# Performance work log

Hardware: AMD Instinct MI355X
Metric: run time of the kernel (lower is better)

## Reference

```python
import jax, jax.numpy as jnp
import numpy as np

N = 50000  # nodes
E = 1600000  # directed edges
F_IN = 64
H = 64
C = 16
EPS = 1e-12


def setup_inputs() -> dict:
    key = jax.random.key(0)
    ks = jax.random.split(key, 10)
    x = jax.random.normal(ks[0], (N, F_IN), jnp.float32)
    edge_index = jax.random.randint(ks[1], (2, E), 0, N, dtype=jnp.int32)
    def lin(k, fan_in, fan_out):
        return jax.random.normal(k, (fan_in, fan_out), jnp.float32) * (1.0 / np.sqrt(fan_in))
    return {
        "x": x,
        "edge_index": edge_index,
        "W1": lin(ks[2], F_IN, H), "b1": jnp.zeros((H,), jnp.float32),
        "W2": lin(ks[3], H, H),    "b2": jnp.zeros((H,), jnp.float32),
        "W3": lin(ks[4], H, H),    "b3": jnp.zeros((H,), jnp.float32),
        "Wlin": lin(ks[5], 3 * H, C), "blin": jnp.zeros((C,), jnp.float32),
    }


def _gcn_norm(edge_index, n):
    # add self loops, compute symmetric GCN normalization D^-1/2 (A+I) D^-1/2
    loop = jnp.arange(n, dtype=edge_index.dtype)
    row = jnp.concatenate([edge_index[0], loop])  # target nodes
    col = jnp.concatenate([edge_index[1], loop])  # source nodes
    deg = jax.ops.segment_sum(jnp.ones_like(row, dtype=jnp.float32), row, num_segments=n)
    dis = jnp.where(deg > 0, jax.lax.rsqrt(jnp.maximum(deg, 1.0)), 0.0)
    norm = dis[row] * dis[col]  # [E+N]
    return row, col, norm


def _gcn_layer(x, row, col, norm, W, b):
    h = x @ W                              # [N, H]
    msg = h[col] * norm[:, None]           # gather sources, scale
    agg = jax.ops.segment_sum(msg, row, num_segments=x.shape[0])  # scatter-add
    return agg + b


def _l2norm(x):
    # torch F.normalize(p=2, dim=1)
    n = jnp.sqrt(jnp.sum(x * x, axis=1, keepdims=True))
    return x / jnp.maximum(n, EPS)


def reference(x, edge_index, W1, b1, W2, b2, W3, b3, Wlin, blin):
    row, col, norm = _gcn_norm(edge_index, x.shape[0])
    stack = []
    h = x
    for (W, b) in ((W1, b1), (W2, b2), (W3, b3)):
        h = _gcn_layer(h, row, col, norm, W, b)
        h = jax.nn.relu(h)
        h = _l2norm(h)
        stack.append(h)
    emb = jnp.concatenate(stack, axis=1)   # [N, 3H]
    out = emb @ Wlin + blin                # [N, C]
    return jax.nn.log_softmax(out, axis=1)
```

## Files before the change

### kernel.cpp

```cpp
#include <hip/hip_runtime.h>
#include <hip/hip_bf16.h>

#define NN 50000
#define NPAD 50048
#define EE 1600000
#define NB 391
#define CAPB 4608
#define CPAD 16
#define EPB 4096
#define BCAP 28

typedef __attribute__((ext_vector_type(8))) short short8;
typedef __attribute__((ext_vector_type(4))) float floatx4;

__device__ __forceinline__ float ldext(const void* p, long i, int f32) {
    return f32 ? ((const float*)p)[i]
               : __bfloat162float(((const __hip_bfloat16*)p)[i]);
}

__device__ __forceinline__ float b2f(unsigned short u) {
    unsigned int x = ((unsigned int)u) << 16;
    float f; __builtin_memcpy(&f, &x, 4); return f;
}
__device__ __forceinline__ unsigned short f2b(float f) {
    __hip_bfloat16 h = __float2bfloat16(f);
    unsigned short u; __builtin_memcpy(&u, &h, 2); return u;
}
__device__ __forceinline__ float asf(unsigned int x) {
    float f; __builtin_memcpy(&f, &x, 4); return f;
}

__global__ void k_bucket(const int* __restrict__ row, const int* __restrict__ col,
                         int* __restrict__ bcur, unsigned int* __restrict__ bdata,
                         const unsigned short* __restrict__ xu, int* __restrict__ flag) {
    __shared__ int lcnt[NB];
    __shared__ unsigned binned[NB * BCAP];
    __shared__ int dcnt;
    int tid = threadIdx.x;
    if (blockIdx.x == 0) {
        if (tid == 0) dcnt = 0;
        __syncthreads();
        int local = 0;
        for (int j = 0; j < 16; ++j) {
            unsigned short u = xu[2 * (tid + 256 * j)];
            int ex = (u >> 7) & 0xFF;
            if (ex == 0xFF || ex < 0x60) local++;
        }
        atomicAdd(&dcnt, local);
        __syncthreads();
        if (tid == 0) flag[0] = (dcnt > 256) ? 1 : 0;
    }
    long base = (long)blockIdx.x * EPB;
    int nedge = (int)min((long)EPB, (long)EE - base);
    for (int k = tid; k < NB; k += 256) lcnt[k] = 0;
    __syncthreads();
    const int4* r4 = (const int4*)(row + base);
    const int4* c4 = (const int4*)(col + base);
    for (int j = tid; j < (nedge >> 2); j += 256) {
        int4 rr = r4[j], cc = c4[j];
        #pragma unroll
        for (int t = 0; t < 4; ++t) {
            int r = (&rr.x)[t], c = (&cc.x)[t];
            int b = r >> 7;
            unsigned rec = ((unsigned)(r & 127) << 16) | (unsigned)c;
            int p = atomicAdd(&lcnt[b], 1);
            if (p < BCAP) binned[b * BCAP + p] = rec;
            else {
                int gp = atomicAdd(&bcur[b * CPAD], 1);
                if (gp < CAPB) bdata[(long)b * CAPB + gp] = rec;
            }
        }
    }
    __syncthreads();
    for (int b = tid; b < NB; b += 256) {
        int n = min(lcnt[b], BCAP);
        if (!n) continue;
        int gb = atomicAdd(&bcur[b * CPAD], n);
        long dst = (long)b * CAPB;
        for (int j = 0; j < n; ++j)
            if (gb + j < CAPB) bdata[dst + gb + j] = binned[b * BCAP + j];
    }
}

__global__ void k_csr(const int* __restrict__ bcur, const unsigned* __restrict__ bdata,
                      int* __restrict__ row_ptr, float* __restrict__ dis,
                      unsigned short* __restrict__ csr_col) {
    __shared__ unsigned recs[CAPB];
    __shared__ int cnt[128];
    __shared__ int incl[128];
    __shared__ int curs[128];
    __shared__ int redu[4];
    int b = blockIdx.x, tid = threadIdx.x;
    int lane = tid & 63, wid = tid >> 6;
    int part = 0;
    for (int j = tid; j < b; j += 256) part += min(bcur[j * CPAD], CAPB);
    #pragma unroll
    for (int off = 32; off; off >>= 1) part += __shfl_xor(part, off);
    if (lane == 0) redu[wid] = part;
    if (tid < 128) cnt[tid] = 0;
    __syncthreads();
    int base = redu[0] + redu[1] + redu[2] + redu[3];
    int n = min(bcur[b * CPAD], CAPB);
    const unsigned* dp = bdata + (long)b * CAPB;
    for (int i = tid; i < n; i += 256) {
        unsigned rec = dp[i];
        recs[i] = rec;
        atomicAdd(&cnt[(rec >> 16) & 127], 1);
    }
    __syncthreads();
    if (tid < 128) {
        int x = cnt[tid];
        #pragma unroll
        for (int off = 1; off < 64; off <<= 1) {
            int y = __shfl_up(x, off);
            if (lane >= off) x += y;
        }
        incl[tid] = x;
    }
    __syncthreads();
    int r0 = b << 7;
    if (tid < 128) {
        int ic = incl[tid] + (wid == 1 ? incl[63] : 0);
        int excl = base + ic - cnt[tid];
        curs[tid] = excl;
        int r = r0 + tid;
        if (r <= NN) row_ptr[r] = excl;
        if (r < NN) dis[r] = rsqrtf((float)(cnt[tid] + 1));
    }
    __syncthreads();
    for (int i = tid; i < n; i += 256) {
        unsigned rec = recs[i];
        int p = atomicAdd(&curs[(rec >> 16) & 127], 1);
        csr_col[p] = (unsigned short)(rec & 0xFFFF);
    }
}

template <bool EXT>
__global__ void k_gemm(const void* __restrict__ X, const void* __restrict__ W,
                       const int* __restrict__ flag, const float* __restrict__ dis,
                       unsigned short* __restrict__ Hout) {
    __shared__ __align__(16) unsigned short xs[64 * 72];
    int tid = threadIdx.x;
    int n0 = blockIdx.x * 64;
    const int f32 = flag[0];
    for (int idx = tid; idx < 4096; idx += 256) {
        int nn = idx >> 6, k = idx & 63;
        int n = n0 + nn;
        unsigned short v = 0;
        if (n < NN) {
            long ofs = (long)n * 64 + k;
            if (EXT) v = f32 ? f2b(((const float*)X)[ofs]) : ((const unsigned short*)X)[ofs];
            else     v = ((const unsigned short*)X)[ofs];
        }
        xs[nn * 72 + k] = v;
    }
    __syncthreads();
    int lane = tid & 63, wid = tid >> 6;
    int m0 = wid * 16;
    int quad = lane >> 4, nl = lane & 15;
    short8 a0 = *(const short8*)(xs + (m0 + nl) * 72 + quad * 8);
    short8 a1 = *(const short8*)(xs + (m0 + nl) * 72 + quad * 8 + 32);
    floatx4 acc[4];
    const unsigned short* Wb = (const unsigned short*)W;
    const float* Wf = (const float*)W;
    #pragma unroll
    for (int ct = 0; ct < 4; ++ct) {
        short8 b0, b1;
        int n = ct * 16 + nl;
        #pragma unroll
        for (int j = 0; j < 8; ++j) {
            int k0 = quad * 8 + j;
            b0[j] = (short)(f32 ? f2b(Wf[k0 * 64 + n]) : Wb[k0 * 64 + n]);
            b1[j] = (short)(f32 ? f2b(Wf[(k0 + 32) * 64 + n]) : Wb[(k0 + 32) * 64 + n]);
        }
        floatx4 c = {0.f, 0.f, 0.f, 0.f};
        c = __builtin_amdgcn_mfma_f32_16x16x32_bf16(a0, b0, c, 0, 0, 0);
        c = __builtin_amdgcn_mfma_f32_16x16x32_bf16(a1, b1, c, 0, 0, 0);
        acc[ct] = c;
    }
    #pragma unroll
    for (int r = 0; r < 4; ++r) {
        int node = n0 + m0 + quad * 4 + r;
        if (node < NN) {
            float dn = dis[node];
            #pragma unroll
            for (int ct = 0; ct < 4; ++ct)
                Hout[(long)node * 64 + ct * 16 + nl] = f2b(dn * acc[ct][r]);
        } else {
            #pragma unroll
            for (int ct = 0; ct < 4; ++ct)
                Hout[(long)node * 64 + ct * 16 + nl] = 0;
        }
    }
}

__global__ void k_agg(const uint4* __restrict__ hp128, const int* __restrict__ row_ptr,
                      const unsigned short* __restrict__ csr_col,
                      const float* __restrict__ dis, const void* __restrict__ bias,
                      const int* __restrict__ flag,
                      unsigned short* __restrict__ eo ) {
    int lane = threadIdx.x & 63, wid = threadIdx.x >> 6;
    int half = lane >> 5;
    int i = blockIdx.x * 8 + wid * 2 + half;
    bool valid = (i < NN);
    int iv = valid ? i : 0;
    int q4 = (lane >> 3) & 3;
    int fl = lane & 7;
    float2 A0 = {0,0}, A1 = {0,0}, A2 = {0,0}, A3 = {0,0};
    #define ADDU(u) do { \
        A0.x += asf((u).x << 16); A0.y += asf((u).x & 0xFFFF0000u); \
        A1.x += asf((u).y << 16); A1.y += asf((u).y & 0xFFFF0000u); \
        A2.x += asf((u).z << 16); A2.y += asf((u).z & 0xFFFF0000u); \
        A3.x += asf((u).w << 16); A3.y += asf((u).w & 0xFFFF0000u); } while (0)
    if (valid && q4 == 0) {
        uint4 u = hp128[(long)iv * 8 + fl];
        ADDU(u);
    }
    int e  = valid ? row_ptr[iv] : 0;
    int e1 = valid ? row_ptr[iv + 1] : 0;
    while (e < e1) {
        int i0 = e + q4,      i1 = e + 4 + q4,  i2 = e + 8 + q4,  i3 = e + 12 + q4;
        int i4 = e + 16 + q4, i5 = e + 20 + q4, i6 = e + 24 + q4, i7 = e + 28 + q4;
        int c0 = (i0 < e1) ? (int)csr_col[i0] : NN;
        int c1 = (i1 < e1) ? (int)csr_col[i1] : NN;
        int c2 = (i2 < e1) ? (int)csr_col[i2] : NN;
        int c3 = (i3 < e1) ? (int)csr_col[i3] : NN;
        int c4 = (i4 < e1) ? (int)csr_col[i4] : NN;
        int c5 = (i5 < e1) ? (int)csr_col[i5] : NN;
        int c6 = (i6 < e1) ? (int)csr_col[i6] : NN;
        int c7 = (i7 < e1) ? (int)csr_col[i7] : NN;
        uint4 u0 = hp128[(long)c0 * 8 + fl];
        uint4 u1 = hp128[(long)c1 * 8 + fl];
        uint4 u2 = hp128[(long)c2 * 8 + fl];
        uint4 u3 = hp128[(long)c3 * 8 + fl];
        uint4 u4 = hp128[(long)c4 * 8 + fl];
        uint4 u5 = hp128[(long)c5 * 8 + fl];
        uint4 u6 = hp128[(long)c6 * 8 + fl];
        uint4 u7 = hp128[(long)c7 * 8 + fl];
        ADDU(u0); ADDU(u1); ADDU(u2); ADDU(u3);
        ADDU(u4); ADDU(u5); ADDU(u6); ADDU(u7);
        e += 32;
    }
    #undef ADDU
    #pragma unroll
    for (int off = 8; off < 32; off <<= 1) {
        A0.x += __shfl_xor(A0.x, off); A0.y += __shfl_xor(A0.y, off);
        A1.x += __shfl_xor(A1.x, off); A1.y += __shfl_xor(A1.y, off);
        A2.x += __shfl_xor(A2.x, off); A2.y += __shfl_xor(A2.y, off);
        A3.x += __shfl_xor(A3.x, off); A3.y += __shfl_xor(A3.y, off);
    }
    const int f32 = flag[0];
    float di = dis[iv];
    float v0 = fmaf(di, A0.x, ldext(bias, 8 * fl + 0, f32));
    float v1 = fmaf(di, A0.y, ldext(bias, 8 * fl + 1, f32));
    float v2 = fmaf(di, A1.x, ldext(bias, 8 * fl + 2, f32));
    float v3 = fmaf(di, A1.y, ldext(bias, 8 * fl + 3, f32));
    float v4 = fmaf(di, A2.x, ldext(bias, 8 * fl + 4, f32));
    float v5 = fmaf(di, A2.y, ldext(bias, 8 * fl + 5, f32));
    float v6 = fmaf(di, A3.x, ldext(bias, 8 * fl + 6, f32));
    float v7 = fmaf(di, A3.y, ldext(bias, 8 * fl + 7, f32));
    v0 = fmaxf(v0, 0.f); v1 = fmaxf(v1, 0.f); v2 = fmaxf(v2, 0.f); v3 = fmaxf(v3, 0.f);
    v4 = fmaxf(v4, 0.f); v5 = fmaxf(v5, 0.f); v6 = fmaxf(v6, 0.f); v7 = fmaxf(v7, 0.f);
    float s = fmaf(v0, v0, fmaf(v1, v1, fmaf(v2, v2, v3 * v3)))
            + fmaf(v4, v4, fmaf(v5, v5, fmaf(v6, v6, v7 * v7)));
    #pragma unroll
    for (int off = 4; off; off >>= 1) s += __shfl_xor(s, off);
    float inv = 1.f / fmaxf(sqrtf(s), 1e-12f);
    if (valid && q4 == 0) {
        union { unsigned short us[8]; uint4 v; } pk;
        pk.us[0] = f2b(v0 * inv); pk.us[1] = f2b(v1 * inv);
        pk.us[2] = f2b(v2 * inv); pk.us[3] = f2b(v3 * inv);
        pk.us[4] = f2b(v4 * inv); pk.us[5] = f2b(v5 * inv);
        pk.us[6] = f2b(v6 * inv); pk.us[7] = f2b(v7 * inv);
        *(uint4*)(eo + (long)i * 64 + 8 * fl) = pk.v;
    }
}

__global__ void k_out(const unsigned short* __restrict__ emb, const void* __restrict__ Wlin,
                      const void* __restrict__ blin, const int* __restrict__ flag,
                      void* __restrict__ out) {
    int tid = threadIdx.x, lane = tid & 63, wid = tid >> 6;
    int quad = lane >> 4, nl = lane & 15;
    int base = blockIdx.x * 64 + wid * 16;
    const int f32 = flag[0];
    const unsigned short* Wb = (const unsigned short*)Wlin;
    const float* Wf = (const float*)Wlin;
    int ia = min(base + nl, NN - 1);
    floatx4 c = {0.f, 0.f, 0.f, 0.f};
    #pragma unroll
    for (int kc = 0; kc < 6; ++kc) {
        short8 b;
        #pragma unroll
        for (int j = 0; j < 8; ++j) {
            int k = kc * 32 + quad * 8 + j;
            b[j] = (short)(f32 ? f2b(Wf[k * 16 + nl]) : Wb[k * 16 + nl]);
        }
        int L = kc >> 1, ko = (kc & 1) * 32 + quad * 8;
        short8 a = *(const short8*)(emb + (long)L * NN * 64 + (long)ia * 64 + ko);
        c = __builtin_amdgcn_mfma_f32_16x16x32_bf16(a, b, c, 0, 0, 0);
    }
    float bl = ldext(blin, nl, f32);
    #pragma unroll
    for (int r = 0; r < 4; ++r) {
        float v = c[r] + bl;
        float m = v;
        #pragma unroll
        for (int off = 1; off < 16; off <<= 1) m = fmaxf(m, __shfl_xor(m, off));
        float ex = __expf(v - m);
        float s = ex;
        #pragma unroll
        for (int off = 1; off < 16; off <<= 1) s += __shfl_xor(s, off);
        float o = (v - m) - __logf(s);
        int node = base + quad * 4 + r;
        if (node < NN) {
            long oidx = (long)node * 16 + nl;
            if (f32) ((float*)out)[oidx] = o;
            else     ((__hip_bfloat16*)out)[oidx] = __float2bfloat16(o);
        }
    }
}

extern "C" void kernel_launch(void* const* d_in, const int* in_sizes, int n_in,
                              void* d_out, int out_size, void* d_ws, size_t ws_size,
                              hipStream_t stream) {
    const void* x    = d_in[0];
    const int*  ei   = (const int*)d_in[1];
    const void* W1   = d_in[2];
    const void* b1   = d_in[3];
    const void* W2   = d_in[4];
    const void* b2   = d_in[5];
    const void* W3   = d_in[6];
    const void* b3   = d_in[7];
    const void* Wlin = d_in[8];
    const void* blin = d_in[9];

    unsigned short* h   = (unsigned short*)d_ws;
    unsigned short* emb = h + (long)NPAD * 64;
    float* dis     = (float*)(emb + (long)3 * NN * 64);
    int*   row_ptr = (int*)(dis + NN);
    int*   flag    = row_ptr + NN + 64;
    int*   bcur    = flag + 16;
    unsigned* bdata = (unsigned*)(bcur + NB * CPAD);
    unsigned short* csr_col = (unsigned short*)(bdata + (long)NB * CAPB);

    const int* row = ei;
    const int* col = ei + EE;

    (void)hipMemsetAsync(bcur, 0, NB * CPAD * sizeof(int), stream);
    k_bucket<<<(EE + EPB - 1) / EPB, 256, 0, stream>>>(row, col, bcur, bdata,
                                                       (const unsigned short*)x, flag);
    k_csr<<<NB, 256, 0, stream>>>(bcur, bdata, row_ptr, dis, csr_col);

    int gb = (NN + 63) / 64;
    int ga = (NN + 7) / 8;
    const uint4* hp128 = (const uint4*)h;
    k_gemm<true><<<gb, 256, 0, stream>>>(x, W1, flag, dis, h);
    k_agg<<<ga, 256, 0, stream>>>(hp128, row_ptr, csr_col, dis, b1, flag, emb);
    k_gemm<false><<<gb, 256, 0, stream>>>(emb, W2, flag, dis, h);
    k_agg<<<ga, 256, 0, stream>>>(hp128, row_ptr, csr_col, dis, b2, flag, emb + (long)NN * 64);
    k_gemm<false><<<gb, 256, 0, stream>>>(emb + (long)NN * 64, W3, flag, dis, h);
    k_agg<<<ga, 256, 0, stream>>>(hp128, row_ptr, csr_col, dis, b3, flag, emb + (long)2 * NN * 64);

    k_out<<<gb, 256, 0, stream>>>(emb, Wlin, blin, flag, d_out);
}
```

Baseline: 299.6 us.

## Split aggregation feature planes across blocks and defer L2 normalization downstream

Each aggregation block now handles one 32-feature half of a node, with paired blocks sharing node groups. That doubles the number of edges gathered concurrently per wavefront (8 edge lanes instead of 4) and uses nontemporal loads for the column indices. The per-node L2 normalization is no longer applied in the aggregation kernel. Instead, partial sums of squares are atomically accumulated into a workspace buffer, and the inverse norm is folded into the next GEMM's row scale and into the output projection per layer. This removes the cross-half reduction dependency but adds atomics, a larger memset, and extra reads of the norm buffer. Unnormalized bf16 embeddings are stored, which may change rounding behaviour.

```diff
diff --git a/kernel.cpp b/kernel.cpp
--- a/kernel.cpp
+++ b/kernel.cpp
@@ -138,6 +138,7 @@
 template <bool EXT>
 __global__ void k_gemm(const void* __restrict__ X, const void* __restrict__ W,
                        const int* __restrict__ flag, const float* __restrict__ dis,
+                       const float* __restrict__ sq,
                        unsigned short* __restrict__ Hout) {
     __shared__ __align__(16) unsigned short xs[64 * 72];
     int tid = threadIdx.x;
@@ -183,6 +184,7 @@
         int node = n0 + m0 + quad * 4 + r;
         if (node < NN) {
             float dn = dis[node];
+            if (!EXT) dn *= 1.f / fmaxf(sqrtf(sq[node]), 1e-12f);
             #pragma unroll
             for (int ct = 0; ct < 4; ++ct)
                 Hout[(long)node * 64 + ct * 16 + nl] = f2b(dn * acc[ct][r]);
@@ -198,52 +200,57 @@
                       const unsigned short* __restrict__ csr_col,
                       const float* __restrict__ dis, const void* __restrict__ bias,
                       const int* __restrict__ flag,
-                      unsigned short* __restrict__ eo ) {
+                      unsigned short* __restrict__ eo ,
+                      float* __restrict__ sq ) {
     int lane = threadIdx.x & 63, wid = threadIdx.x >> 6;
+    int bid = blockIdx.x;
+    int plane = (bid >> 2) & 1;
+    int grp = (bid >> 3) * 4 + (bid & 3);
     int half = lane >> 5;
-    int i = blockIdx.x * 8 + wid * 2 + half;
+    int i = grp * 8 + wid * 2 + half;
     bool valid = (i < NN);
     int iv = valid ? i : 0;
-    int q4 = (lane >> 3) & 3;
-    int fl = lane & 7;
+    int q  = (lane >> 2) & 7;
+    int fl = lane & 3;
+    const int fo = plane * 4 + fl;
     float2 A0 = {0,0}, A1 = {0,0}, A2 = {0,0}, A3 = {0,0};
     #define ADDU(u) do { \
         A0.x += asf((u).x << 16); A0.y += asf((u).x & 0xFFFF0000u); \
         A1.x += asf((u).y << 16); A1.y += asf((u).y & 0xFFFF0000u); \
         A2.x += asf((u).z << 16); A2.y += asf((u).z & 0xFFFF0000u); \
         A3.x += asf((u).w << 16); A3.y += asf((u).w & 0xFFFF0000u); } while (0)
-    if (valid && q4 == 0) {
-        uint4 u = hp128[(long)iv * 8 + fl];
+    if (valid && q == 0) {
+        uint4 u = hp128[(long)iv * 8 + fo];
         ADDU(u);
     }
     int e  = valid ? row_ptr[iv] : 0;
     int e1 = valid ? row_ptr[iv + 1] : 0;
     while (e < e1) {
-        int i0 = e + q4,      i1 = e + 4 + q4,  i2 = e + 8 + q4,  i3 = e + 12 + q4;
-        int i4 = e + 16 + q4, i5 = e + 20 + q4, i6 = e + 24 + q4, i7 = e + 28 + q4;
-        int c0 = (i0 < e1) ? (int)csr_col[i0] : NN;
-        int c1 = (i1 < e1) ? (int)csr_col[i1] : NN;
-        int c2 = (i2 < e1) ? (int)csr_col[i2] : NN;
-        int c3 = (i3 < e1) ? (int)csr_col[i3] : NN;
-        int c4 = (i4 < e1) ? (int)csr_col[i4] : NN;
-        int c5 = (i5 < e1) ? (int)csr_col[i5] : NN;
-        int c6 = (i6 < e1) ? (int)csr_col[i6] : NN;
-        int c7 = (i7 < e1) ? (int)csr_col[i7] : NN;
-        uint4 u0 = hp128[(long)c0 * 8 + fl];
-        uint4 u1 = hp128[(long)c1 * 8 + fl];
-        uint4 u2 = hp128[(long)c2 * 8 + fl];
-        uint4 u3 = hp128[(long)c3 * 8 + fl];
-        uint4 u4 = hp128[(long)c4 * 8 + fl];
-        uint4 u5 = hp128[(long)c5 * 8 + fl];
-        uint4 u6 = hp128[(long)c6 * 8 + fl];
-        uint4 u7 = hp128[(long)c7 * 8 + fl];
+        int i0 = e + q,      i1 = e + 8 + q,  i2 = e + 16 + q, i3 = e + 24 + q;
+        int i4 = e + 32 + q, i5 = e + 40 + q, i6 = e + 48 + q, i7 = e + 56 + q;
+        int c0 = (i0 < e1) ? (int)__builtin_nontemporal_load(csr_col + i0) : NN;
+        int c1 = (i1 < e1) ? (int)__builtin_nontemporal_load(csr_col + i1) : NN;
+        int c2 = (i2 < e1) ? (int)__builtin_nontemporal_load(csr_col + i2) : NN;
+        int c3 = (i3 < e1) ? (int)__builtin_nontemporal_load(csr_col + i3) : NN;
+        int c4 = (i4 < e1) ? (int)__builtin_nontemporal_load(csr_col + i4) : NN;
+        int c5 = (i5 < e1) ? (int)__builtin_nontemporal_load(csr_col + i5) : NN;
+        int c6 = (i6 < e1) ? (int)__builtin_nontemporal_load(csr_col + i6) : NN;
+        int c7 = (i7 < e1) ? (int)__builtin_nontemporal_load(csr_col + i7) : NN;
+        uint4 u0 = hp128[(long)c0 * 8 + fo];
+        uint4 u1 = hp128[(long)c1 * 8 + fo];
+        uint4 u2 = hp128[(long)c2 * 8 + fo];
+        uint4 u3 = hp128[(long)c3 * 8 + fo];
+        uint4 u4 = hp128[(long)c4 * 8 + fo];
+        uint4 u5 = hp128[(long)c5 * 8 + fo];
+        uint4 u6 = hp128[(long)c6 * 8 + fo];
+        uint4 u7 = hp128[(long)c7 * 8 + fo];
         ADDU(u0); ADDU(u1); ADDU(u2); ADDU(u3);
         ADDU(u4); ADDU(u5); ADDU(u6); ADDU(u7);
-        e += 32;
+        e += 64;
     }
     #undef ADDU
     #pragma unroll
-    for (int off = 8; off < 32; off <<= 1) {
+    for (int off = 4; off < 32; off <<= 1) {
         A0.x += __shfl_xor(A0.x, off); A0.y += __shfl_xor(A0.y, off);
         A1.x += __shfl_xor(A1.x, off); A1.y += __shfl_xor(A1.y, off);
         A2.x += __shfl_xor(A2.x, off); A2.y += __shfl_xor(A2.y, off);
@@ -251,33 +258,35 @@
     }
     const int f32 = flag[0];
     float di = dis[iv];
-    float v0 = fmaf(di, A0.x, ldext(bias, 8 * fl + 0, f32));
-    float v1 = fmaf(di, A0.y, ldext(bias, 8 * fl + 1, f32));
-    float v2 = fmaf(di, A1.x, ldext(bias, 8 * fl + 2, f32));
-    float v3 = fmaf(di, A1.y, ldext(bias, 8 * fl + 3, f32));
-    float v4 = fmaf(di, A2.x, ldext(bias, 8 * fl + 4, f32));
-    float v5 = fmaf(di, A2.y, ldext(bias, 8 * fl + 5, f32));
-    float v6 = fmaf(di, A3.x, ldext(bias, 8 * fl + 6, f32));
-    float v7 = fmaf(di, A3.y, ldext(bias, 8 * fl + 7, f32));
+    int fb = plane * 32 + fl * 8;
+    float v0 = fmaf(di, A0.x, ldext(bias, fb + 0, f32));
+    float v1 = fmaf(di, A0.y, ldext(bias, fb + 1, f32));
+    float v2 = fmaf(di, A1.x, ldext(bias, fb + 2, f32));
+    float v3 = fmaf(di, A1.y, ldext(bias, fb + 3, f32));
+    float v4 = fmaf(di, A2.x, ldext(bias, fb + 4, f32));
+    float v5 = fmaf(di, A2.y, ldext(bias, fb + 5, f32));
+    float v6 = fmaf(di, A3.x, ldext(bias, fb + 6, f32));
+    float v7 = fmaf(di, A3.y, ldext(bias, fb + 7, f32));
     v0 = fmaxf(v0, 0.f); v1 = fmaxf(v1, 0.f); v2 = fmaxf(v2, 0.f); v3 = fmaxf(v3, 0.f);
     v4 = fmaxf(v4, 0.f); v5 = fmaxf(v5, 0.f); v6 = fmaxf(v6, 0.f); v7 = fmaxf(v7, 0.f);
     float s = fmaf(v0, v0, fmaf(v1, v1, fmaf(v2, v2, v3 * v3)))
             + fmaf(v4, v4, fmaf(v5, v5, fmaf(v6, v6, v7 * v7)));
-    #pragma unroll
-    for (int off = 4; off; off >>= 1) s += __shfl_xor(s, off);
-    float inv = 1.f / fmaxf(sqrtf(s), 1e-12f);
-    if (valid && q4 == 0) {
+    s += __shfl_xor(s, 1);
+    s += __shfl_xor(s, 2);
+    if (valid && q == 0) {
         union { unsigned short us[8]; uint4 v; } pk;
-        pk.us[0] = f2b(v0 * inv); pk.us[1] = f2b(v1 * inv);
-        pk.us[2] = f2b(v2 * inv); pk.us[3] = f2b(v3 * inv);
-        pk.us[4] = f2b(v4 * inv); pk.us[5] = f2b(v5 * inv);
-        pk.us[6] = f2b(v6 * inv); pk.us[7] = f2b(v7 * inv);
-        *(uint4*)(eo + (long)i * 64 + 8 * fl) = pk.v;
+        pk.us[0] = f2b(v0); pk.us[1] = f2b(v1);
+        pk.us[2] = f2b(v2); pk.us[3] = f2b(v3);
+        pk.us[4] = f2b(v4); pk.us[5] = f2b(v5);
+        pk.us[6] = f2b(v6); pk.us[7] = f2b(v7);
+        *(uint4*)(eo + (long)i * 64 + fb) = pk.v;
+        if (fl == 0) atomicAdd(&sq[i], s);
     }
 }
 
 __global__ void k_out(const unsigned short* __restrict__ emb, const void* __restrict__ Wlin,
                       const void* __restrict__ blin, const int* __restrict__ flag,
+                      const float* __restrict__ sumsq ,
                       void* __restrict__ out) {
     int tid = threadIdx.x, lane = tid & 63, wid = tid >> 6;
     int quad = lane >> 4, nl = lane & 15;
@@ -286,33 +295,41 @@
     const unsigned short* Wb = (const unsigned short*)Wlin;
     const float* Wf = (const float*)Wlin;
     int ia = min(base + nl, NN - 1);
-    floatx4 c = {0.f, 0.f, 0.f, 0.f};
-    #pragma unroll
-    for (int kc = 0; kc < 6; ++kc) {
-        short8 b;
+    floatx4 cL[3];
+    #pragma unroll
+    for (int L = 0; L < 3; ++L) cL[L] = floatx4{0.f, 0.f, 0.f, 0.f};
+    #pragma unroll
+    for (int L = 0; L < 3; ++L) {
         #pragma unroll
-        for (int j = 0; j < 8; ++j) {
-            int k = kc * 32 + quad * 8 + j;
-            b[j] = (short)(f32 ? f2b(Wf[k * 16 + nl]) : Wb[k * 16 + nl]);
-        }
-        int L = kc >> 1, ko = (kc & 1) * 32 + quad * 8;
-        short8 a = *(const short8*)(emb + (long)L * NN * 64 + (long)ia * 64 + ko);
-        c = __builtin_amdgcn_mfma_f32_16x16x32_bf16(a, b, c, 0, 0, 0);
+        for (int kh = 0; kh < 2; ++kh) {
+            short8 b;
+            #pragma unroll
+            for (int j = 0; j < 8; ++j) {
+                int k = L * 64 + kh * 32 + quad * 8 + j;
+                b[j] = (short)(f32 ? f2b(Wf[k * 16 + nl]) : Wb[k * 16 + nl]);
+            }
+            int ko = kh * 32 + quad * 8;
+            short8 a = *(const short8*)(emb + (long)L * NN * 64 + (long)ia * 64 + ko);
+            cL[L] = __builtin_amdgcn_mfma_f32_16x16x32_bf16(a, b, cL[L], 0, 0, 0);
+        }
     }
     float bl = ldext(blin, nl, f32);
     #pragma unroll
     for (int r = 0; r < 4; ++r) {
-        float v = c[r] + bl;
-        float m = v;
-        #pragma unroll
-        for (int off = 1; off < 16; off <<= 1) m = fmaxf(m, __shfl_xor(m, off));
-        float ex = __expf(v - m);
-        float s = ex;
-        #pragma unroll
-        for (int off = 1; off < 16; off <<= 1) s += __shfl_xor(s, off);
-        float o = (v - m) - __logf(s);
         int node = base + quad * 4 + r;
         if (node < NN) {
+            float i0 = 1.f / fmaxf(sqrtf(sumsq[node]), 1e-12f);
+            float i1 = 1.f / fmaxf(sqrtf(sumsq[NN + node]), 1e-12f);
+            float i2 = 1.f / fmaxf(sqrtf(sumsq[2 * NN + node]), 1e-12f);
+            float v = fmaf(i0, cL[0][r], fmaf(i1, cL[1][r], fmaf(i2, cL[2][r], bl)));
+            float m = v;
+            #pragma unroll
+            for (int off = 1; off < 16; off <<= 1) m = fmaxf(m, __shfl_xor(m, off));
+            float ex = __expf(v - m);
+            float s = ex;
+            #pragma unroll
+            for (int off = 1; off < 16; off <<= 1) s += __shfl_xor(s, off);
+            float o = (v - m) - __logf(s);
             long oidx = (long)node * 16 + nl;
             if (f32) ((float*)out)[oidx] = o;
             else     ((__hip_bfloat16*)out)[oidx] = __float2bfloat16(o);
@@ -339,27 +356,32 @@
     float* dis     = (float*)(emb + (long)3 * NN * 64);
     int*   row_ptr = (int*)(dis + NN);
     int*   flag    = row_ptr + NN + 64;
-    int*   bcur    = flag + 16;
+    float* sumsq   = (float*)(flag + 16);
+    int*   bcur    = (int*)(sumsq + 3 * NN);
     unsigned* bdata = (unsigned*)(bcur + NB * CPAD);
     unsigned short* csr_col = (unsigned short*)(bdata + (long)NB * CAPB);
 
     const int* row = ei;
     const int* col = ei + EE;
 
-    (void)hipMemsetAsync(bcur, 0, NB * CPAD * sizeof(int), stream);
+    (void)hipMemsetAsync(sumsq, 0, (3 * NN + NB * CPAD) * sizeof(int), stream);
     k_bucket<<<(EE + EPB - 1) / EPB, 256, 0, stream>>>(row, col, bcur, bdata,
                                                        (const unsigned short*)x, flag);
     k_csr<<<NB, 256, 0, stream>>>(bcur, bdata, row_ptr, dis, csr_col);
 
     int gb = (NN + 63) / 64;
-    int ga = (NN + 7) / 8;
+    int ga = 1563 * 8;
     const uint4* hp128 = (const uint4*)h;
-    k_gemm<true><<<gb, 256, 0, stream>>>(x, W1, flag, dis, h);
-    k_agg<<<ga, 256, 0, stream>>>(hp128, row_ptr, csr_col, dis, b1, flag, emb);
-    k_gemm<false><<<gb, 256, 0, stream>>>(emb, W2, flag, dis, h);
-    k_agg<<<ga, 256, 0, stream>>>(hp128, row_ptr, csr_col, dis, b2, flag, emb + (long)NN * 64);
-    k_gemm<false><<<gb, 256, 0, stream>>>(emb + (long)NN * 64, W3, flag, dis, h);
-    k_agg<<<ga, 256, 0, stream>>>(hp128, row_ptr, csr_col, dis, b3, flag, emb + (long)2 * NN * 64);
-
-    k_out<<<gb, 256, 0, stream>>>(emb, Wlin, blin, flag, d_out);
-}
+    k_gemm<true><<<gb, 256, 0, stream>>>(x, W1, flag, dis, nullptr, h);
+    k_agg<<<ga, 256, 0, stream>>>(hp128, row_ptr, csr_col, dis, b1, flag,
+                                  emb, sumsq);
+    k_gemm<false><<<gb, 256, 0, stream>>>(emb, W2, flag, dis, sumsq, h);
+    k_agg<<<ga, 256, 0, stream>>>(hp128, row_ptr, csr_col, dis, b2, flag,
+                                  emb + (long)NN * 64, sumsq + NN);
+    k_gemm<false><<<gb, 256, 0, stream>>>(emb + (long)NN * 64, W3, flag, dis,
+                                          sumsq + NN, h);
+    k_agg<<<ga, 256, 0, stream>>>(hp128, row_ptr, csr_col, dis, b3, flag,
+                                  emb + (long)2 * NN * 64, sumsq + 2 * NN);
+
+    k_out<<<gb, 256, 0, stream>>>(emb, Wlin, blin, flag, sumsq, d_out);
+}
```

Result: slower. 357.7 us (+19.4%).

## Pad CSR rows to 32 entries, vectorize index loads, stage W in LDS

Applied to the files above, without the earlier changes.

The CSR builder now pads each row's neighbor list to a multiple of 32 with a sentinel (NN) and gives each bucket a fixed PBCAP slot region. This removes the global prefix sum over buckets and lets the aggregation kernel load 8 column indices with one 16-byte load, with no bounds checks. The GEMM kernel stages W transposed in shared memory once per block, replacing the scattered per-lane global loads of W. The costs are extra CSR memory and wasted gathers on padded sentinel entries. Rows that overflow PBCAP would be silently truncated.

```diff
diff --git a/kernel.cpp b/kernel.cpp
--- a/kernel.cpp
+++ b/kernel.cpp
@@ -9,6 +9,7 @@
 #define CPAD 16
 #define EPB 4096
 #define BCAP 28
+#define PBCAP 7424
 
 typedef __attribute__((ext_vector_type(8))) short short8;
 typedef __attribute__((ext_vector_type(4))) float floatx4;
@@ -18,10 +19,6 @@
                : __bfloat162float(((const __hip_bfloat16*)p)[i]);
 }
 
-__device__ __forceinline__ float b2f(unsigned short u) {
-    unsigned int x = ((unsigned int)u) << 16;
-    float f; __builtin_memcpy(&f, &x, 4); return f;
-}
 __device__ __forceinline__ unsigned short f2b(float f) {
     __hip_bfloat16 h = __float2bfloat16(f);
     unsigned short u; __builtin_memcpy(&u, &h, 2); return u;
@@ -83,23 +80,16 @@
 }
 
 __global__ void k_csr(const int* __restrict__ bcur, const unsigned* __restrict__ bdata,
-                      int* __restrict__ row_ptr, float* __restrict__ dis,
-                      unsigned short* __restrict__ csr_col) {
+                      int* __restrict__ rp0, int* __restrict__ degA,
+                      float* __restrict__ dis, unsigned short* __restrict__ csr_col) {
     __shared__ unsigned recs[CAPB];
     __shared__ int cnt[128];
     __shared__ int incl[128];
     __shared__ int curs[128];
-    __shared__ int redu[4];
     int b = blockIdx.x, tid = threadIdx.x;
     int lane = tid & 63, wid = tid >> 6;
-    int part = 0;
-    for (int j = tid; j < b; j += 256) part += min(bcur[j * CPAD], CAPB);
-    #pragma unroll
-    for (int off = 32; off; off >>= 1) part += __shfl_xor(part, off);
-    if (lane == 0) redu[wid] = part;
     if (tid < 128) cnt[tid] = 0;
     __syncthreads();
-    int base = redu[0] + redu[1] + redu[2] + redu[3];
     int n = min(bcur[b * CPAD], CAPB);
     const unsigned* dp = bdata + (long)b * CAPB;
     for (int i = tid; i < n; i += 256) {
@@ -109,7 +99,7 @@
     }
     __syncthreads();
     if (tid < 128) {
-        int x = cnt[tid];
+        int x = (cnt[tid] + 31) & ~31;
         #pragma unroll
         for (int off = 1; off < 64; off <<= 1) {
             int y = __shfl_up(x, off);
@@ -119,19 +109,27 @@
     }
     __syncthreads();
     int r0 = b << 7;
+    int lim = (b + 1) * PBCAP;
     if (tid < 128) {
+        int c = cnt[tid];
+        int x = (c + 31) & ~31;
         int ic = incl[tid] + (wid == 1 ? incl[63] : 0);
-        int excl = base + ic - cnt[tid];
+        int excl = b * PBCAP + ic - x;
         curs[tid] = excl;
         int r = r0 + tid;
-        if (r <= NN) row_ptr[r] = excl;
-        if (r < NN) dis[r] = rsqrtf((float)(cnt[tid] + 1));
+        if (r < NN) {
+            rp0[r] = excl;
+            degA[r] = c;
+            dis[r] = rsqrtf((float)(c + 1));
+        }
+        for (int j = c; j < x && excl + j < lim; ++j)
+            csr_col[excl + j] = (unsigned short)NN;
     }
     __syncthreads();
     for (int i = tid; i < n; i += 256) {
         unsigned rec = recs[i];
         int p = atomicAdd(&curs[(rec >> 16) & 127], 1);
-        csr_col[p] = (unsigned short)(rec & 0xFFFF);
+        if (p < lim) csr_col[p] = (unsigned short)(rec & 0xFFFF);
     }
 }
 
@@ -140,9 +138,12 @@
                        const int* __restrict__ flag, const float* __restrict__ dis,
                        unsigned short* __restrict__ Hout) {
     __shared__ __align__(16) unsigned short xs[64 * 72];
+    __shared__ __align__(16) unsigned short ws[64 * 72];
     int tid = threadIdx.x;
     int n0 = blockIdx.x * 64;
     const int f32 = flag[0];
+    const unsigned short* Wb = (const unsigned short*)W;
+    const float* Wf = (const float*)W;
     for (int idx = tid; idx < 4096; idx += 256) {
         int nn = idx >> 6, k = idx & 63;
         int n = n0 + nn;
@@ -153,6 +154,8 @@
             else     v = ((const unsigned short*)X)[ofs];
         }
         xs[nn * 72 + k] = v;
+        int wk = idx >> 6, wn = idx & 63;
+        ws[wn * 72 + wk] = f32 ? f2b(Wf[idx]) : Wb[idx];
     }
     __syncthreads();
     int lane = tid & 63, wid = tid >> 6;
@@ -161,18 +164,11 @@
     short8 a0 = *(const short8*)(xs + (m0 + nl) * 72 + quad * 8);
     short8 a1 = *(const short8*)(xs + (m0 + nl) * 72 + quad * 8 + 32);
     floatx4 acc[4];
-    const unsigned short* Wb = (const unsigned short*)W;
-    const float* Wf = (const float*)W;
     #pragma unroll
     for (int ct = 0; ct < 4; ++ct) {
-        short8 b0, b1;
         int n = ct * 16 + nl;
-        #pragma unroll
-        for (int j = 0; j < 8; ++j) {
-            int k0 = quad * 8 + j;
-            b0[j] = (short)(f32 ? f2b(Wf[k0 * 64 + n]) : Wb[k0 * 64 + n]);
-            b1[j] = (short)(f32 ? f2b(Wf[(k0 + 32) * 64 + n]) : Wb[(k0 + 32) * 64 + n]);
-        }
+        short8 b0 = *(const short8*)(ws + n * 72 + quad * 8);
+        short8 b1 = *(const short8*)(ws + n * 72 + quad * 8 + 32);
         floatx4 c = {0.f, 0.f, 0.f, 0.f};
         c = __builtin_amdgcn_mfma_f32_16x16x32_bf16(a0, b0, c, 0, 0, 0);
         c = __builtin_amdgcn_mfma_f32_16x16x32_bf16(a1, b1, c, 0, 0, 0);
@@ -194,10 +190,10 @@
     }
 }
 
-__global__ void k_agg(const uint4* __restrict__ hp128, const int* __restrict__ row_ptr,
+__global__ void k_agg(const uint4* __restrict__ hp128, const int* __restrict__ rp0,
+                      const int* __restrict__ degA, const float* __restrict__ dis,
                       const unsigned short* __restrict__ csr_col,
-                      const float* __restrict__ dis, const void* __restrict__ bias,
-                      const int* __restrict__ flag,
+                      const void* __restrict__ bias, const int* __restrict__ flag,
                       unsigned short* __restrict__ eo ) {
     int lane = threadIdx.x & 63, wid = threadIdx.x >> 6;
     int half = lane >> 5;
@@ -216,19 +212,15 @@
         uint4 u = hp128[(long)iv * 8 + fl];
         ADDU(u);
     }
-    int e  = valid ? row_ptr[iv] : 0;
-    int e1 = valid ? row_ptr[iv + 1] : 0;
-    while (e < e1) {
-        int i0 = e + q4,      i1 = e + 4 + q4,  i2 = e + 8 + q4,  i3 = e + 12 + q4;
-        int i4 = e + 16 + q4, i5 = e + 20 + q4, i6 = e + 24 + q4, i7 = e + 28 + q4;
-        int c0 = (i0 < e1) ? (int)csr_col[i0] : NN;
-        int c1 = (i1 < e1) ? (int)csr_col[i1] : NN;
-        int c2 = (i2 < e1) ? (int)csr_col[i2] : NN;
-        int c3 = (i3 < e1) ? (int)csr_col[i3] : NN;
-        int c4 = (i4 < e1) ? (int)csr_col[i4] : NN;
-        int c5 = (i5 < e1) ? (int)csr_col[i5] : NN;
-        int c6 = (i6 < e1) ? (int)csr_col[i6] : NN;
-        int c7 = (i7 < e1) ? (int)csr_col[i7] : NN;
+    int e0 = rp0[iv];
+    int pd = (degA[iv] + 31) & ~31;
+    const unsigned short* cb = csr_col + e0 + q4 * 8;
+    for (int t = 0; t < pd; t += 32) {
+        uint4 I = *(const uint4*)(cb + t);
+        int c0 = (int)(I.x & 0xFFFFu), c1 = (int)(I.x >> 16);
+        int c2 = (int)(I.y & 0xFFFFu), c3 = (int)(I.y >> 16);
+        int c4 = (int)(I.z & 0xFFFFu), c5 = (int)(I.z >> 16);
+        int c6 = (int)(I.w & 0xFFFFu), c7 = (int)(I.w >> 16);
         uint4 u0 = hp128[(long)c0 * 8 + fl];
         uint4 u1 = hp128[(long)c1 * 8 + fl];
         uint4 u2 = hp128[(long)c2 * 8 + fl];
@@ -239,7 +231,6 @@
         uint4 u7 = hp128[(long)c7 * 8 + fl];
         ADDU(u0); ADDU(u1); ADDU(u2); ADDU(u3);
         ADDU(u4); ADDU(u5); ADDU(u6); ADDU(u7);
-        e += 32;
     }
     #undef ADDU
     #pragma unroll
@@ -337,8 +328,9 @@
     unsigned short* h   = (unsigned short*)d_ws;
     unsigned short* emb = h + (long)NPAD * 64;
     float* dis     = (float*)(emb + (long)3 * NN * 64);
-    int*   row_ptr = (int*)(dis + NN);
-    int*   flag    = row_ptr + NN + 64;
+    int*   rp0     = (int*)(dis + NN);
+    int*   degA    = rp0 + NN;
+    int*   flag    = degA + NN;
     int*   bcur    = flag + 16;
     unsigned* bdata = (unsigned*)(bcur + NB * CPAD);
     unsigned short* csr_col = (unsigned short*)(bdata + (long)NB * CAPB);
@@ -349,17 +341,19 @@
     (void)hipMemsetAsync(bcur, 0, NB * CPAD * sizeof(int), stream);
     k_bucket<<<(EE + EPB - 1) / EPB, 256, 0, stream>>>(row, col, bcur, bdata,
                                                        (const unsigned short*)x, flag);
-    k_csr<<<NB, 256, 0, stream>>>(bcur, bdata, row_ptr, dis, csr_col);
+    k_csr<<<NB, 256, 0, stream>>>(bcur, bdata, rp0, degA, dis, csr_col);
 
     int gb = (NN + 63) / 64;
     int ga = (NN + 7) / 8;
     const uint4* hp128 = (const uint4*)h;
     k_gemm<true><<<gb, 256, 0, stream>>>(x, W1, flag, dis, h);
-    k_agg<<<ga, 256, 0, stream>>>(hp128, row_ptr, csr_col, dis, b1, flag, emb);
+    k_agg<<<ga, 256, 0, stream>>>(hp128, rp0, degA, dis, csr_col, b1, flag, emb);
     k_gemm<false><<<gb, 256, 0, stream>>>(emb, W2, flag, dis, h);
-    k_agg<<<ga, 256, 0, stream>>>(hp128, row_ptr, csr_col, dis, b2, flag, emb + (long)NN * 64);
+    k_agg<<<ga, 256, 0, stream>>>(hp128, rp0, degA, dis, csr_col, b2, flag,
+                                  emb + (long)NN * 64);
     k_gemm<false><<<gb, 256, 0, stream>>>(emb + (long)NN * 64, W3, flag, dis, h);
-    k_agg<<<ga, 256, 0, stream>>>(hp128, row_ptr, csr_col, dis, b3, flag, emb + (long)2 * NN * 64);
+    k_agg<<<ga, 256, 0, stream>>>(hp128, rp0, degA, dis, csr_col, b3, flag,
+                                  emb + (long)2 * NN * 64);
 
     k_out<<<gb, 256, 0, stream>>>(emb, Wlin, blin, flag, d_out);
 }
```

Result: faster. 273.1 us (-8.8%).
